# Kernel tuning notes

Hardware: AMD Instinct MI355X
Metric: run time of the kernel (lower is better)

Reference implementation:

```python
import jax, jax.numpy as jnp
import numpy as np

HIDDEN = 2048
NUM_HEADS = 32
NUM_KV_HEADS = 8
HEAD_DIM = 64
ROPE_THETA = 10000.0


def _rope_tables(S, dtype=jnp.float32):
    freqs = 1.0 / (ROPE_THETA ** (jnp.arange(0, HEAD_DIM, 2, dtype=jnp.float32) / HEAD_DIM))
    angles = jnp.arange(S, dtype=jnp.float32)[:, None] * freqs[None, :]  # [S, D/2]
    return jnp.cos(angles).astype(dtype), jnp.sin(angles).astype(dtype)


def _apply_rope(x, cos, sin):
    # x: [B, H, S, D] with interleaved even/odd rotation pairs
    xe = x[..., 0::2]
    xo = x[..., 1::2]
    oe = xe * cos - xo * sin
    oo = xe * sin + xo * cos
    return jnp.stack([oe, oo], axis=-1).reshape(x.shape)


def setup_inputs() -> dict:
    key = jax.random.key(0)
    ks = jax.random.split(key, 5)
    scale = 0.02
    return {
        "x": jax.random.normal(ks[0], (2, 2048, HIDDEN), dtype=jnp.float32),
        "wq": jax.random.normal(ks[1], (NUM_HEADS * HEAD_DIM, HIDDEN), dtype=jnp.float32) * scale,
        "wk": jax.random.normal(ks[2], (NUM_KV_HEADS * HEAD_DIM, HIDDEN), dtype=jnp.float32) * scale,
        "wv": jax.random.normal(ks[3], (NUM_KV_HEADS * HEAD_DIM, HIDDEN), dtype=jnp.float32) * scale,
        "wo": jax.random.normal(ks[4], (HIDDEN, NUM_HEADS * HEAD_DIM), dtype=jnp.float32) * scale,
    }


def reference(x, wq, wk, wv, wo):
    B, S, _ = x.shape
    G = NUM_HEADS // NUM_KV_HEADS  # GQA group size

    q = (x @ wq.T).reshape(B, S, NUM_HEADS, HEAD_DIM).transpose(0, 2, 1, 3)      # [B,Hq,S,D]
    k = (x @ wk.T).reshape(B, S, NUM_KV_HEADS, HEAD_DIM).transpose(0, 2, 1, 3)   # [B,Hkv,S,D]
    v = (x @ wv.T).reshape(B, S, NUM_KV_HEADS, HEAD_DIM).transpose(0, 2, 1, 3)

    cos, sin = _rope_tables(S, x.dtype)
    q = _apply_rope(q, cos, sin)
    k = _apply_rope(k, cos, sin)

    # GQA without materializing repeated K/V: fold group dim into q
    qg = q.reshape(B, NUM_KV_HEADS, G, S, HEAD_DIM)
    scale = 1.0 / jnp.sqrt(jnp.asarray(HEAD_DIM, dtype=x.dtype))
    scores = jnp.einsum("bkgsd,bktd->bkgst", qg, k) * scale  # [B,Hkv,G,S,S]

    causal = jnp.tril(jnp.ones((S, S), dtype=bool))
    scores = jnp.where(causal, scores, jnp.finfo(scores.dtype).min)
    probs = jax.nn.softmax(scores, axis=-1)

    out = jnp.einsum("bkgst,bktd->bkgsd", probs, v)                 # [B,Hkv,G,S,D]
    out = out.reshape(B, NUM_HEADS, S, HEAD_DIM).transpose(0, 2, 1, 3).reshape(B, S, NUM_HEADS * HEAD_DIM)
    return out @ wo.T
```

## Files before the change

### kernel.cpp

```cpp
#include <hip/hip_runtime.h>
#include <hip/hip_bf16.h>

typedef __hip_bfloat16 bf16;
typedef __attribute__((ext_vector_type(8))) short short8;
typedef __attribute__((ext_vector_type(4))) float f32x4;

#define S_LEN 2048
#define BATCH 2
#define M_TOT 4096
#define HID 2048
#define NH 32
#define NKV 8
#define HD 64
#define KVD 512

#define MFMA16(a, b, c) __builtin_amdgcn_mfma_f32_16x16x32_bf16(a, b, c, 0, 0, 0)

__device__ __forceinline__ void gload_lds16(const bf16* g, bf16* l) {
    __builtin_amdgcn_global_load_lds((const __attribute__((address_space(1))) void*)g,
                                     (__attribute__((address_space(3))) void*)l,
                                     16, 0, 0);
}

__device__ __forceinline__ float b2f(short v) {
    unsigned u = ((unsigned)(unsigned short)v) << 16;
    float f; __builtin_memcpy(&f, &u, 4); return f;
}

#define N8_X   1048576
#define N8_WQ   524288
#define N8_WK   131072
#define N8_TOT 2359296
__global__ void cast_all_kernel(const float* __restrict__ x, const float* __restrict__ wq,
                                const float* __restrict__ wk, const float* __restrict__ wv,
                                const float* __restrict__ wo, bf16* __restrict__ dst) {
    int stride = gridDim.x * blockDim.x;
    for (int i = blockIdx.x * blockDim.x + threadIdx.x; i < N8_TOT; i += stride) {
        const float* s; int off;
        if (i < N8_X)                        { s = x;  off = i; }
        else if (i < N8_X + N8_WQ)           { s = wq; off = i - N8_X; }
        else if (i < N8_X + N8_WQ + N8_WK)   { s = wk; off = i - (N8_X + N8_WQ); }
        else if (i < N8_X + N8_WQ + 2*N8_WK) { s = wv; off = i - (N8_X + N8_WQ + N8_WK); }
        else                                 { s = wo; off = i - (N8_X + N8_WQ + 2*N8_WK); }
        const float4* sp = (const float4*)(s + (size_t)off * 8);
        float4 a = sp[0], b = sp[1];
        bf16 tmp[8];
        tmp[0] = __float2bfloat16(a.x); tmp[1] = __float2bfloat16(a.y);
        tmp[2] = __float2bfloat16(a.z); tmp[3] = __float2bfloat16(a.w);
        tmp[4] = __float2bfloat16(b.x); tmp[5] = __float2bfloat16(b.y);
        tmp[6] = __float2bfloat16(b.z); tmp[7] = __float2bfloat16(b.w);
        *(short8*)(dst + (size_t)i * 8) = *(short8*)tmp;
    }
}

__global__ void rope_tables_kernel(float* __restrict__ cosb, float* __restrict__ sinb) {
    int idx = blockIdx.x * blockDim.x + threadIdx.x;
    if (idx >= S_LEN * 32) return;
    int s = idx >> 5, d = idx & 31;
    float freq = powf(10000.0f, -(float)(2 * d) / 64.0f);
    float ang = (float)s * freq;
    cosb[idx] = cosf(ang);
    sinb[idx] = sinf(ang);
}

__global__ void rope_kernel(bf16* __restrict__ buf, const float* __restrict__ cosb,
                            const float* __restrict__ sinb, int nh, int npairs) {
    int stride = gridDim.x * blockDim.x;
    int hw = nh * 32;
    for (int idx = blockIdx.x * blockDim.x + threadIdx.x; idx < npairs; idx += stride) {
        int m = idx / hw;
        int r = idx - m * hw;
        int h = r >> 5, d = r & 31;
        int s = m & (S_LEN - 1);
        float c = cosb[s * 32 + d], sn = sinb[s * 32 + d];
        bf16* p = buf + (size_t)m * (nh * HD) + h * HD + 2 * d;
        __hip_bfloat162 xv = *(__hip_bfloat162*)p;
        float xe = __bfloat162float(xv.x), xo = __bfloat162float(xv.y);
        __hip_bfloat162 ov;
        ov.x = __float2bfloat16(xe * c - xo * sn);
        ov.y = __float2bfloat16(xe * sn + xo * c);
        *(__hip_bfloat162*)p = ov;
    }
}

__device__ __forceinline__ short8 rope8(short8 v, float4 c, float4 s) {
    short8 o;
    const float* cp = (const float*)&c;
    const float* sp = (const float*)&s;
    #pragma unroll
    for (int m = 0; m < 4; m++) {
        float xe = b2f(v[2 * m]) * 0.125f;
        float xo = b2f(v[2 * m + 1]) * 0.125f;
        bf16 oe = __float2bfloat16(xe * cp[m] - xo * sp[m]);
        bf16 oo = __float2bfloat16(xe * sp[m] + xo * cp[m]);
        short se, so;
        __builtin_memcpy(&se, &oe, 2); __builtin_memcpy(&so, &oo, 2);
        o[2 * m] = se; o[2 * m + 1] = so;
    }
    return o;
}

__device__ __forceinline__ void gemm_core(const bf16* __restrict__ A,
                                          const bf16* __restrict__ W,
                                          int K, int m0, int n0,
                                          bf16* As, bf16* Bs,
                                          f32x4 acc[4][4]) {
    int tid = threadIdx.x;
    int lane = tid & 63, wid = tid >> 6;
    int wr = wid >> 1, wc = wid & 1;
    int lhi = lane >> 4, llo = lane & 15;
    int c0 = tid, c1 = tid + 256;
    int r0 = c0 >> 2, s0 = ((c0 & 3) ^ (r0 & 3)) * 8;
    int r1 = c1 >> 2, s1 = ((c1 & 3) ^ (r1 & 3)) * 8;
    const bf16* gA0 = A + (size_t)(m0 + r0) * K + s0;
    const bf16* gA1 = A + (size_t)(m0 + r1) * K + s1;
    const bf16* gB0 = W + (size_t)(n0 + r0) * K + s0;
    const bf16* gB1 = W + (size_t)(n0 + r1) * K + s1;

    auto stage = [&](int buf, int k0) {
        bf16* a = As + buf * 4096;
        bf16* b = Bs + buf * 4096;
        gload_lds16(gA0 + k0, a + c0 * 8);
        gload_lds16(gA1 + k0, a + c1 * 8);
        gload_lds16(gB0 + k0, b + c0 * 8);
        gload_lds16(gB1 + k0, b + c1 * 8);
    };

    stage(0, 0);
    asm volatile("s_waitcnt vmcnt(0)" ::: "memory");
    __builtin_amdgcn_s_barrier();
    int buf = 0;
    for (int k0 = 0; k0 < K; k0 += 32) {
        if (k0 + 32 < K) stage(buf ^ 1, k0 + 32);
        const bf16* Ac = As + buf * 4096;
        const bf16* Bc = Bs + buf * 4096;
        short8 af[4], bfr[4];
        #pragma unroll
        for (int i = 0; i < 4; i++) {
            int row = wr * 64 + i * 16 + llo;
            af[i] = *(const short8*)(Ac + row * 32 + ((lhi ^ (row & 3)) * 8));
        }
        #pragma unroll
        for (int j = 0; j < 4; j++) {
            int row = wc * 64 + j * 16 + llo;
            bfr[j] = *(const short8*)(Bc + row * 32 + ((lhi ^ (row & 3)) * 8));
        }
        #pragma unroll
        for (int i = 0; i < 4; i++)
            #pragma unroll
            for (int j = 0; j < 4; j++)
                acc[i][j] = MFMA16(af[i], bfr[j], acc[i][j]);
        asm volatile("s_waitcnt vmcnt(0)" ::: "memory");
        __builtin_amdgcn_s_barrier();
        buf ^= 1;
    }
}

__global__ __launch_bounds__(256) void gemm_qkv_kernel(
        const bf16* __restrict__ xb,
        const bf16* __restrict__ wq, const bf16* __restrict__ wk, const bf16* __restrict__ wv,
        bf16* __restrict__ qb, bf16* __restrict__ kb, bf16* __restrict__ vtb) {
    __shared__ bf16 As[2 * 128 * 32];
    __shared__ bf16 Bs[2 * 128 * 32];
    int by = blockIdx.y;
    const bf16* W; bf16* Cb; int n0, ldc, mode;
    if (by < 16)      { W = wq; Cb = qb;  n0 = by * 128;        ldc = 2048; mode = 0; }
    else if (by < 20) { W = wk; Cb = kb;  n0 = (by - 16) * 128; ldc = 512;  mode = 0; }
    else              { W = wv; Cb = vtb; n0 = (by - 20) * 128; ldc = 0;    mode = 1; }
    int bx = blockIdx.x;
    int bxs = (bx & 7) * 4 + (bx >> 3);
    int m0 = bxs * 128;

    f32x4 acc[4][4] = {};
    gemm_core(xb, W, HID, m0, n0, As, Bs, acc);

    int lane = threadIdx.x & 63, wid = threadIdx.x >> 6;
    int wr = wid >> 1, wc = wid & 1;
    int lhi = lane >> 4, llo = lane & 15;
    #pragma unroll
    for (int i = 0; i < 4; i++)
        #pragma unroll
        for (int j = 0; j < 4; j++) {
            int col = wc * 64 + j * 16 + llo;
            #pragma unroll
            for (int r = 0; r < 4; r++) {
                int row = wr * 64 + i * 16 + lhi * 4 + r;
                int m = m0 + row;
                float v = acc[i][j][r];
                if (mode == 0) {
                    Cb[(size_t)m * ldc + n0 + col] = __float2bfloat16(v);
                } else {
                    int bb = m >> 11, ss = m & 2047;
                    Cb[((size_t)(bb * 512 + n0 + col)) * S_LEN + ss] = __float2bfloat16(v);
                }
            }
        }
}

__global__ __launch_bounds__(256) void gemm_out_kernel(
        const bf16* __restrict__ attnb, const bf16* __restrict__ wob,
        float* __restrict__ out) {
    __shared__ bf16 As[2 * 128 * 32];
    __shared__ bf16 Bs[2 * 128 * 32];
    int bx = blockIdx.x;
    int bxs = (bx & 7) * 4 + (bx >> 3);
    int m0 = bxs * 128;
    int n0 = blockIdx.y * 128;
    f32x4 acc[4][4] = {};
    gemm_core(attnb, wob, HID, m0, n0, As, Bs, acc);

    int lane = threadIdx.x & 63, wid = threadIdx.x >> 6;
    int wr = wid >> 1, wc = wid & 1;
    int lhi = lane >> 4, llo = lane & 15;
    #pragma unroll
    for (int i = 0; i < 4; i++)
        #pragma unroll
        for (int j = 0; j < 4; j++) {
            int col = wc * 64 + j * 16 + llo;
            #pragma unroll
            for (int r = 0; r < 4; r++) {
                int row = wr * 64 + i * 16 + lhi * 4 + r;
                out[(size_t)(m0 + row) * HID + n0 + col] = acc[i][j][r];
            }
        }
}

__global__ __launch_bounds__(256, 4) void flash_kernel(
        const bf16* __restrict__ qb, const bf16* __restrict__ kb,
        const bf16* __restrict__ vtb, const float* __restrict__ cosb,
        const float* __restrict__ sinb, bf16* __restrict__ attnb) {
    __shared__ bf16 Ks[2][64 * 64];
    __shared__ bf16 Vs[2][64 * 64];
    __shared__ bf16 Pl[4][16 * 64];
    int bh = blockIdx.y;
    int b = bh >> 5, h = bh & 31;
    int kvh = h >> 2;
    int tid = threadIdx.x;
    int wid = tid >> 6, lane = tid & 63;
    int lhi = lane >> 4, llo = lane & 15;

    const bf16* Kg = kb + (size_t)(b * S_LEN) * KVD + kvh * HD;
    const bf16* Vg = vtb + (size_t)(b * 512 + kvh * 64) * S_LEN;

    int c0 = tid, c1 = tid + 256;
    int r0 = c0 >> 3, s0 = ((c0 & 7) ^ (r0 & 7)) * 8;
    int r1 = c1 >> 3, s1 = ((c1 & 7) ^ (r1 & 7)) * 8;

    bf16* pl = &Pl[wid][0];
    const int prd0 = llo * 64 + ((lhi ^ (llo & 7)) * 8);
    const int prd1 = llo * 64 + (((lhi + 4) ^ (llo & 7)) * 8);

    auto stage = [&](int buf, int t0) {
        gload_lds16(Kg + (size_t)(t0 + r0) * KVD + s0, &Ks[buf][c0 * 8]);
        gload_lds16(Kg + (size_t)(t0 + r1) * KVD + s1, &Ks[buf][c1 * 8]);
        gload_lds16(Vg + (size_t)r0 * S_LEN + t0 + s0, &Vs[buf][c0 * 8]);
        gload_lds16(Vg + (size_t)r1 * S_LEN + t0 + s1, &Vs[buf][c1 * 8]);
    };

    auto run_phase = [&](int j) {
        int qrow0 = j * 64 + wid * 16;
        int spos = qrow0 + llo;
        const bf16* qrow = qb + ((size_t)(b * S_LEN) + spos) * (NH * HD) + h * HD;
        float4 cv0 = *(const float4*)(cosb + spos * 32 + lhi * 4);
        float4 sv0 = *(const float4*)(sinb + spos * 32 + lhi * 4);
        float4 cv1 = *(const float4*)(cosb + spos * 32 + 16 + lhi * 4);
        float4 sv1 = *(const float4*)(sinb + spos * 32 + 16 + lhi * 4);
        short8 qf0 = rope8(*(const short8*)(qrow + lhi * 8), cv0, sv0);
        short8 qf1 = rope8(*(const short8*)(qrow + 32 + lhi * 8), cv1, sv1);

        f32x4 acc[4] = {};
        float psum[4] = {0.f, 0.f, 0.f, 0.f};

        stage(0, 0);
        asm volatile("s_waitcnt vmcnt(0)" ::: "memory");
        __builtin_amdgcn_s_barrier();
        int cur = 0;
        for (int t = 0; t <= j; ++t) {
            int t0 = t * 64;
            if (t < j) stage(cur ^ 1, t0 + 64);
            const bf16* Kc = &Ks[cur][0];
            const bf16* Vc = &Vs[cur][0];
            f32x4 z[4];
            #pragma unroll
            for (int cb = 0; cb < 4; cb++) {
                int row = cb * 16 + llo;
                int x = row & 7;
                short8 k0 = *(const short8*)(Kc + row * 64 + ((lhi ^ x) * 8));
                short8 k1 = *(const short8*)(Kc + row * 64 + (((lhi + 4) ^ x) * 8));
                f32x4 zz = {0.f, 0.f, 0.f, 0.f};
                zz = MFMA16(qf0, k0, zz);
                zz = MFMA16(qf1, k1, zz);
                z[cb] = zz;
            }
            if (t == j) {
                #pragma unroll
                for (int cb = 0; cb < 4; cb++)
                    #pragma unroll
                    for (int r = 0; r < 4; r++) {
                        float p = __expf(z[cb][r]);
                        p = (t0 + cb * 16 + llo <= qrow0 + lhi * 4 + r) ? p : 0.f;
                        psum[r] += p;
                        int row = lhi * 4 + r;
                        pl[row * 64 + (((2 * cb + (llo >> 3)) ^ (row & 7)) * 8) + (llo & 7)]
                            = __float2bfloat16(p);
                    }
            } else {
                #pragma unroll
                for (int cb = 0; cb < 4; cb++)
                    #pragma unroll
                    for (int r = 0; r < 4; r++) {
                        float p = __expf(z[cb][r]);
                        psum[r] += p;
                        int row = lhi * 4 + r;
                        pl[row * 64 + (((2 * cb + (llo >> 3)) ^ (row & 7)) * 8) + (llo & 7)]
                            = __float2bfloat16(p);
                    }
            }
            short8 pa0 = *(const short8*)(pl + prd0);
            short8 pa1 = *(const short8*)(pl + prd1);
            #pragma unroll
            for (int jb = 0; jb < 4; jb++) {
                int row = jb * 16 + llo;
                int x = row & 7;
                short8 v0 = *(const short8*)(Vc + row * 64 + ((lhi ^ x) * 8));
                short8 v1 = *(const short8*)(Vc + row * 64 + (((lhi + 4) ^ x) * 8));
                acc[jb] = MFMA16(pa0, v0, acc[jb]);
                acc[jb] = MFMA16(pa1, v1, acc[jb]);
            }
            asm volatile("s_waitcnt vmcnt(0)" ::: "memory");
            __builtin_amdgcn_s_barrier();
            cur ^= 1;
        }
        #pragma unroll
        for (int off = 1; off < 16; off <<= 1)
            #pragma unroll
            for (int r = 0; r < 4; r++)
                psum[r] += __shfl_xor(psum[r], off, 64);
        float inv[4];
        #pragma unroll
        for (int r = 0; r < 4; r++) inv[r] = 1.0f / psum[r];
        size_t obase = ((size_t)(b * S_LEN) + qrow0) * (NH * HD) + h * HD;
        #pragma unroll
        for (int jb = 0; jb < 4; jb++)
            #pragma unroll
            for (int r = 0; r < 4; r++)
                attnb[obase + (size_t)(lhi * 4 + r) * (NH * HD) + jb * 16 + llo] =
                    __float2bfloat16(acc[jb][r] * inv[r]);
    };

    run_phase(blockIdx.x);
    run_phase(31 - blockIdx.x);
}

extern "C" void kernel_launch(void* const* d_in, const int* in_sizes, int n_in,
                              void* d_out, int out_size, void* d_ws, size_t ws_size,
                              hipStream_t stream) {
    const float* x  = (const float*)d_in[0];
    const float* wq = (const float*)d_in[1];
    const float* wk = (const float*)d_in[2];
    const float* wv = (const float*)d_in[3];
    const float* wo = (const float*)d_in[4];
    float* out = (float*)d_out;

    char* ws = (char*)d_ws;
    size_t off = 0;
    auto alloc = [&](size_t bytes) { void* p = ws + off; off += (bytes + 255) & ~(size_t)255; return p; };
    bf16* xb   = (bf16*)alloc((size_t)M_TOT * HID * 2);
    bf16* wqb  = (bf16*)alloc((size_t)HID * HID * 2);
    bf16* wkb  = (bf16*)alloc((size_t)512 * HID * 2);
    bf16* wvb  = (bf16*)alloc((size_t)512 * HID * 2);
    bf16* wob  = (bf16*)alloc((size_t)HID * HID * 2);
    bf16* qb   = (bf16*)alloc((size_t)M_TOT * 2048 * 2);
    bf16* kb   = (bf16*)alloc((size_t)M_TOT * 512 * 2);
    bf16* vtb  = (bf16*)alloc((size_t)M_TOT * 512 * 2);
    bf16* attnb= (bf16*)alloc((size_t)M_TOT * 2048 * 2);
    float* cosb= (float*)alloc((size_t)S_LEN * 32 * 4);
    float* sinb= (float*)alloc((size_t)S_LEN * 32 * 4);

    cast_all_kernel<<<2048, 256, 0, stream>>>(x, wq, wk, wv, wo, xb);

    rope_tables_kernel<<<(S_LEN * 32 + 255) / 256, 256, 0, stream>>>(cosb, sinb);

    gemm_qkv_kernel<<<dim3(M_TOT / 128, 24), 256, 0, stream>>>(xb, wqb, wkb, wvb, qb, kb, vtb);

    {
        int npairs = M_TOT * NKV * 32;
        rope_kernel<<<(npairs + 255) / 256, 256, 0, stream>>>(kb, cosb, sinb, NKV, npairs);
    }

    flash_kernel<<<dim3(16, BATCH * NH), 256, 0, stream>>>(qb, kb, vtb, cosb, sinb, attnb);

    gemm_out_kernel<<<dim3(M_TOT / 128, HID / 128), 256, 0, stream>>>(attnb, wob, out);
}
```

Baseline: 215.0 us.

## Triple-buffer GEMM LDS pipeline, change swizzle, vectorize K RoPE kernel

The shared GEMM core now uses three LDS stages with two tiles in flight. It waits with vmcnt(4) instead of draining all loads each iteration, so global loads overlap more with MFMA work. The LDS XOR swizzle now keys on (row>>1)&3 to change the bank-conflict pattern of the 16-byte fragment reads. The per-pair K RoPE kernel is replaced by a vectorized version that processes 8 bf16 per thread with float4 cos/sin loads. The cost is 50% more LDS per GEMM block, which may reduce occupancy.

```diff
diff --git a/kernel.cpp b/kernel.cpp
--- a/kernel.cpp
+++ b/kernel.cpp
@@ -63,34 +63,14 @@
     sinb[idx] = sinf(ang);
 }
 
-__global__ void rope_kernel(bf16* __restrict__ buf, const float* __restrict__ cosb,
-                            const float* __restrict__ sinb, int nh, int npairs) {
-    int stride = gridDim.x * blockDim.x;
-    int hw = nh * 32;
-    for (int idx = blockIdx.x * blockDim.x + threadIdx.x; idx < npairs; idx += stride) {
-        int m = idx / hw;
-        int r = idx - m * hw;
-        int h = r >> 5, d = r & 31;
-        int s = m & (S_LEN - 1);
-        float c = cosb[s * 32 + d], sn = sinb[s * 32 + d];
-        bf16* p = buf + (size_t)m * (nh * HD) + h * HD + 2 * d;
-        __hip_bfloat162 xv = *(__hip_bfloat162*)p;
-        float xe = __bfloat162float(xv.x), xo = __bfloat162float(xv.y);
-        __hip_bfloat162 ov;
-        ov.x = __float2bfloat16(xe * c - xo * sn);
-        ov.y = __float2bfloat16(xe * sn + xo * c);
-        *(__hip_bfloat162*)p = ov;
-    }
-}
-
-__device__ __forceinline__ short8 rope8(short8 v, float4 c, float4 s) {
+__device__ __forceinline__ short8 rope8(short8 v, float4 c, float4 s, float scale) {
     short8 o;
     const float* cp = (const float*)&c;
     const float* sp = (const float*)&s;
     #pragma unroll
     for (int m = 0; m < 4; m++) {
-        float xe = b2f(v[2 * m]) * 0.125f;
-        float xo = b2f(v[2 * m + 1]) * 0.125f;
+        float xe = b2f(v[2 * m]) * scale;
+        float xo = b2f(v[2 * m + 1]) * scale;
         bf16 oe = __float2bfloat16(xe * cp[m] - xo * sp[m]);
         bf16 oo = __float2bfloat16(xe * sp[m] + xo * cp[m]);
         short se, so;
@@ -98,6 +78,21 @@
         o[2 * m] = se; o[2 * m + 1] = so;
     }
     return o;
+}
+
+__global__ void rope_k_kernel(bf16* __restrict__ buf, const float* __restrict__ cosb,
+                              const float* __restrict__ sinb) {
+    int idx = blockIdx.x * blockDim.x + threadIdx.x;
+    if (idx >= M_TOT * 64) return;
+    int m = idx >> 6, c = idx & 63;
+    int e0 = c * 8;
+    int d0 = (e0 & 63) >> 1;
+    int s = m & (S_LEN - 1);
+    bf16* p = buf + (size_t)m * KVD + e0;
+    short8 v = *(const short8*)p;
+    float4 cv = *(const float4*)(cosb + s * 32 + d0);
+    float4 sv = *(const float4*)(sinb + s * 32 + d0);
+    *(short8*)p = rope8(v, cv, sv, 1.0f);
 }
 
 __device__ __forceinline__ void gemm_core(const bf16* __restrict__ A,
@@ -110,8 +105,8 @@
     int wr = wid >> 1, wc = wid & 1;
     int lhi = lane >> 4, llo = lane & 15;
     int c0 = tid, c1 = tid + 256;
-    int r0 = c0 >> 2, s0 = ((c0 & 3) ^ (r0 & 3)) * 8;
-    int r1 = c1 >> 2, s1 = ((c1 & 3) ^ (r1 & 3)) * 8;
+    int r0 = c0 >> 2, s0 = ((c0 & 3) ^ ((r0 >> 1) & 3)) * 8;
+    int r1 = c1 >> 2, s1 = ((c1 & 3) ^ ((r1 >> 1) & 3)) * 8;
     const bf16* gA0 = A + (size_t)(m0 + r0) * K + s0;
     const bf16* gA1 = A + (size_t)(m0 + r1) * K + s1;
     const bf16* gB0 = W + (size_t)(n0 + r0) * K + s0;
@@ -125,43 +120,49 @@
         gload_lds16(gB0 + k0, b + c0 * 8);
         gload_lds16(gB1 + k0, b + c1 * 8);
     };
-
-    stage(0, 0);
-    asm volatile("s_waitcnt vmcnt(0)" ::: "memory");
-    __builtin_amdgcn_s_barrier();
-    int buf = 0;
-    for (int k0 = 0; k0 < K; k0 += 32) {
-        if (k0 + 32 < K) stage(buf ^ 1, k0 + 32);
+    auto compute = [&](int buf) {
         const bf16* Ac = As + buf * 4096;
         const bf16* Bc = Bs + buf * 4096;
         short8 af[4], bfr[4];
         #pragma unroll
         for (int i = 0; i < 4; i++) {
             int row = wr * 64 + i * 16 + llo;
-            af[i] = *(const short8*)(Ac + row * 32 + ((lhi ^ (row & 3)) * 8));
+            af[i] = *(const short8*)(Ac + row * 32 + ((lhi ^ ((row >> 1) & 3)) * 8));
         }
         #pragma unroll
         for (int j = 0; j < 4; j++) {
             int row = wc * 64 + j * 16 + llo;
-            bfr[j] = *(const short8*)(Bc + row * 32 + ((lhi ^ (row & 3)) * 8));
+            bfr[j] = *(const short8*)(Bc + row * 32 + ((lhi ^ ((row >> 1) & 3)) * 8));
         }
         #pragma unroll
         for (int i = 0; i < 4; i++)
             #pragma unroll
             for (int j = 0; j < 4; j++)
                 acc[i][j] = MFMA16(af[i], bfr[j], acc[i][j]);
-        asm volatile("s_waitcnt vmcnt(0)" ::: "memory");
+    };
+
+    int nt = K / 32;
+    stage(0, 0);
+    stage(1, 32);
+    int b0 = 0, b1 = 1, b2 = 2;
+    for (int t = 0; t < nt - 1; ++t) {
+        asm volatile("s_waitcnt vmcnt(4)" ::: "memory");
         __builtin_amdgcn_s_barrier();
-        buf ^= 1;
+        compute(b0);
+        if (t + 2 < nt) stage(b2, (t + 2) * 32);
+        int tmp = b0; b0 = b1; b1 = b2; b2 = tmp;
     }
+    asm volatile("s_waitcnt vmcnt(0)" ::: "memory");
+    __builtin_amdgcn_s_barrier();
+    compute(b0);
 }
 
 __global__ __launch_bounds__(256) void gemm_qkv_kernel(
         const bf16* __restrict__ xb,
         const bf16* __restrict__ wq, const bf16* __restrict__ wk, const bf16* __restrict__ wv,
         bf16* __restrict__ qb, bf16* __restrict__ kb, bf16* __restrict__ vtb) {
-    __shared__ bf16 As[2 * 128 * 32];
-    __shared__ bf16 Bs[2 * 128 * 32];
+    __shared__ bf16 As[3 * 128 * 32];
+    __shared__ bf16 Bs[3 * 128 * 32];
     int by = blockIdx.y;
     const bf16* W; bf16* Cb; int n0, ldc, mode;
     if (by < 16)      { W = wq; Cb = qb;  n0 = by * 128;        ldc = 2048; mode = 0; }
@@ -200,8 +201,8 @@
 __global__ __launch_bounds__(256) void gemm_out_kernel(
         const bf16* __restrict__ attnb, const bf16* __restrict__ wob,
         float* __restrict__ out) {
-    __shared__ bf16 As[2 * 128 * 32];
-    __shared__ bf16 Bs[2 * 128 * 32];
+    __shared__ bf16 As[3 * 128 * 32];
+    __shared__ bf16 Bs[3 * 128 * 32];
     int bx = blockIdx.x;
     int bxs = (bx & 7) * 4 + (bx >> 3);
     int m0 = bxs * 128;
@@ -265,8 +266,8 @@
         float4 sv0 = *(const float4*)(sinb + spos * 32 + lhi * 4);
         float4 cv1 = *(const float4*)(cosb + spos * 32 + 16 + lhi * 4);
         float4 sv1 = *(const float4*)(sinb + spos * 32 + 16 + lhi * 4);
-        short8 qf0 = rope8(*(const short8*)(qrow + lhi * 8), cv0, sv0);
-        short8 qf1 = rope8(*(const short8*)(qrow + 32 + lhi * 8), cv1, sv1);
+        short8 qf0 = rope8(*(const short8*)(qrow + lhi * 8), cv0, sv0, 0.125f);
+        short8 qf1 = rope8(*(const short8*)(qrow + 32 + lhi * 8), cv1, sv1, 0.125f);
 
         f32x4 acc[4] = {};
         float psum[4] = {0.f, 0.f, 0.f, 0.f};
@@ -383,10 +384,7 @@
 
     gemm_qkv_kernel<<<dim3(M_TOT / 128, 24), 256, 0, stream>>>(xb, wqb, wkb, wvb, qb, kb, vtb);
 
-    {
-        int npairs = M_TOT * NKV * 32;
-        rope_kernel<<<(npairs + 255) / 256, 256, 0, stream>>>(kb, cosb, sinb, NKV, npairs);
-    }
+    rope_k_kernel<<<(M_TOT * 64 + 255) / 256, 256, 0, stream>>>(kb, cosb, sinb);
 
     flash_kernel<<<dim3(16, BATCH * NH), 256, 0, stream>>>(qb, kb, vtb, cosb, sinb, attnb);
 
```

After: 198.3 us. 1.08x faster.
